# Optimization experiments

Measured on AMD Instinct MI355X. Metric: run time of the kernel, lower is better.

The kernel has to match this reference:

```python
import jax, jax.numpy as jnp
import numpy as np

HIDDEN = 1024  # must match init_kwargs hidden_size


def setup_inputs() -> dict:
    key = jax.random.key(0)
    k1, k2 = jax.random.split(key)
    B, SQ, SKV, D = 4, 4096, 4096, HIDDEN
    query = jax.random.normal(k1, (B, SQ, D), dtype=jnp.float32)
    key_value_states = jax.random.normal(k2, (B, SKV, D), dtype=jnp.float32)
    attention_mask = jnp.zeros((B, 1, SKV), dtype=jnp.float32)
    return {
        "query": query,
        "key_value_states": key_value_states,
        "attention_mask": attention_mask,
        "layer_idx": 0,
    }


def reference(query, key_value_states, attention_mask, layer_idx):
    # compression_rate = 1.0 + layer_idx/12*3 ; layer_idx=0 -> rate 1.0 (no compression)
    scale = 1.0 / jnp.sqrt(jnp.asarray(HIDDEN, dtype=query.dtype))
    # scores: [B, Sq, Skv]
    scores = jnp.einsum("bqd,bkd->bqk", query, key_value_states) * scale
    scores = scores + attention_mask
    attn = jax.nn.softmax(scores, axis=-1)
    # dropout is identity (eval / p=0)
    out = jnp.einsum("bqk,bkd->bqd", attn, key_value_states)
    return out, attn
```

## Files before the change

kernel.cpp:

```cpp
#include <hip/hip_runtime.h>
#include <stdint.h>

#define B_   4
#define SQ_  4096
#define SKV_ 4096
#define D_   1024

typedef __attribute__((ext_vector_type(4))) float f32x4;
typedef __attribute__((ext_vector_type(8))) short bf8_t;

__device__ __forceinline__ unsigned short f2bf(float f) {
    unsigned u = __float_as_uint(f);
    u += 0x7fff + ((u >> 16) & 1);
    return (unsigned short)(u >> 16);
}

__device__ __forceinline__ void gload_lds16(const void* g, void* l) {
    __builtin_amdgcn_global_load_lds(
        (const __attribute__((address_space(1))) unsigned int*)g,
        (__attribute__((address_space(3))) unsigned int*)l,
        16, 0, 0);
}

__device__ __forceinline__ void barrier_mem() {
    asm volatile("" ::: "memory");
    __builtin_amdgcn_s_barrier();
    asm volatile("" ::: "memory");
}

__global__ void cvt_f32_bf16_kernel(const float* __restrict__ in,
                                    unsigned short* __restrict__ out, int n4) {
    int stride = gridDim.x * blockDim.x;
    for (int i = blockIdx.x * blockDim.x + threadIdx.x; i < n4; i += stride) {
        float4 v = ((const float4*)in)[i];
        ushort4 o;
        o.x = f2bf(v.x); o.y = f2bf(v.y); o.z = f2bf(v.z); o.w = f2bf(v.w);
        ((ushort4*)out)[i] = o;
    }
}

__global__ void transpose_cvt_kernel(const float* __restrict__ V,
                                     unsigned short* __restrict__ VT) {
    __shared__ float tile[32][33];
    int b = blockIdx.z;
    const float* Vb = V + (size_t)b * SKV_ * D_;
    unsigned short* VTb = VT + (size_t)b * D_ * SKV_;
    int d0 = blockIdx.x * 32, k0 = blockIdx.y * 32;
    int x = threadIdx.x, y = threadIdx.y;
    #pragma unroll
    for (int i = 0; i < 4; ++i)
        tile[y + i * 8][x] = Vb[(size_t)(k0 + y + i * 8) * D_ + d0 + x];
    __syncthreads();
    #pragma unroll
    for (int i = 0; i < 4; ++i)
        VTb[(size_t)(d0 + y + i * 8) * SKV_ + k0 + x] = f2bf(tile[x][y + i * 8]);
}

__global__ __launch_bounds__(512, 2) void gemm256_nt_bf16_kernel(
    const unsigned short* __restrict__ A, int lda, size_t strideA,
    const unsigned short* __restrict__ Bm, int ldb, size_t strideB,
    float* __restrict__ C, int ldc, size_t strideC,
    int K, float scale, const float* __restrict__ mask)
{
    __shared__ __align__(16) unsigned char smem[131072];

    const int tid  = threadIdx.x;
    const int lane = tid & 63, wid = tid >> 6;
    const int wr = wid >> 2, wc = wid & 3;

    int lin  = blockIdx.y * gridDim.x + blockIdx.x;
    int q8   = (gridDim.x * gridDim.y) >> 3;
    int lin2 = (lin & 7) * q8 + (lin >> 3);
    int bn = lin2 % gridDim.x, bm = lin2 / gridDim.x;
    int bz = blockIdx.z;

    const char* Ab = (const char*)(A + (size_t)bz * strideA);
    const char* Bb = (const char*)(Bm + (size_t)bz * strideB);
    float* Cb = C + (size_t)bz * strideC;
    const int ldaB = lda * 2, ldbB = ldb * 2;

    const int srow = ((tid >> 6) * 16) + (tid & 15);
    const int scol = ((tid >> 4) & 3) * 16;
    const char* Apan = Ab + (size_t)(bm * 256 + srow) * ldaB + scol;
    const char* Bpan = Bb + (size_t)(bn * 256 + srow) * ldbB + scol;
    char* ldsA = (char*)smem;
    char* ldsB = (char*)smem + 65536;

    const char* aRd = (char*)smem + wr * 8192 + lane * 16;
    const char* bRd = (char*)smem + 65536 + wc * 4096 + lane * 16;

    f32x4 acc[8][4] = {};
    const int NT = K >> 6;

#define STAGE_A(tt, hh) do { \
    const char* s_ = Apan + (tt) * 128 + (hh) * 64; \
    char* d_ = ldsA + (((tt) & 1) * 32768) + (hh) * 16384 + tid * 16; \
    gload_lds16(s_, d_); \
    gload_lds16(s_ + (size_t)128 * ldaB, d_ + 8192); \
} while (0)
#define STAGE_B(tt, hh) do { \
    const char* s_ = Bpan + (tt) * 128 + (hh) * 64; \
    char* d_ = ldsB + (((tt) & 1) * 32768) + (hh) * 16384 + tid * 16; \
    gload_lds16(s_, d_); \
    gload_lds16(s_ + (size_t)128 * ldbB, d_ + 8192); \
} while (0)

    STAGE_A(0, 0); STAGE_A(0, 1); STAGE_B(0, 0); STAGE_B(0, 1);
    if (NT > 1) {
        STAGE_A(1, 0); STAGE_B(1, 0); STAGE_B(1, 1);
        asm volatile("s_waitcnt vmcnt(6)" ::: "memory");
    } else {
        asm volatile("s_waitcnt vmcnt(0)" ::: "memory");
    }
    barrier_mem();

    for (int t = 0; t < NT; ++t) {
        const int p = t & 1;
        const char* aT = aRd + p * 32768;
        const char* bT = bRd + p * 32768;
        bf8_t a0[8], a1[8], b0[4], b1[4];

        #pragma unroll
        for (int m = 0; m < 8; ++m) a0[m] = *(const bf8_t*)(aT + m * 1024);
        #pragma unroll
        for (int n = 0; n < 4; ++n) b0[n] = *(const bf8_t*)(bT + n * 1024);
        if (t + 1 < NT) STAGE_A(t + 1, 1);
        barrier_mem();
        __builtin_amdgcn_s_setprio(1);
        #pragma unroll
        for (int m = 0; m < 4; ++m)
            #pragma unroll
            for (int n = 0; n < 4; ++n)
                acc[m][n] = __builtin_amdgcn_mfma_f32_16x16x32_bf16(a0[m], b0[n], acc[m][n], 0, 0, 0);
        __builtin_amdgcn_s_setprio(0);
        barrier_mem();

        #pragma unroll
        for (int n = 0; n < 4; ++n) b1[n] = *(const bf8_t*)(bT + 16384 + n * 1024);
        if (t + 2 < NT) STAGE_A(t + 2, 0);
        barrier_mem();
        __builtin_amdgcn_s_setprio(1);
        #pragma unroll
        for (int m = 0; m < 4; ++m)
            #pragma unroll
            for (int n = 0; n < 4; ++n)
                acc[m + 4][n] = __builtin_amdgcn_mfma_f32_16x16x32_bf16(a0[m + 4], b0[n], acc[m + 4][n], 0, 0, 0);
        __builtin_amdgcn_s_setprio(0);
        barrier_mem();

        #pragma unroll
        for (int m = 0; m < 8; ++m) a1[m] = *(const bf8_t*)(aT + 16384 + m * 1024);
        if (t + 2 < NT) STAGE_B(t + 2, 0);
        barrier_mem();
        __builtin_amdgcn_s_setprio(1);
        #pragma unroll
        for (int m = 0; m < 4; ++m)
            #pragma unroll
            for (int n = 0; n < 4; ++n)
                acc[m][n] = __builtin_amdgcn_mfma_f32_16x16x32_bf16(a1[m], b1[n], acc[m][n], 0, 0, 0);
        __builtin_amdgcn_s_setprio(0);
        barrier_mem();

        if (t + 2 < NT) STAGE_B(t + 2, 1);
        barrier_mem();
        __builtin_amdgcn_s_setprio(1);
        #pragma unroll
        for (int m = 0; m < 4; ++m)
            #pragma unroll
            for (int n = 0; n < 4; ++n)
                acc[m + 4][n] = __builtin_amdgcn_mfma_f32_16x16x32_bf16(a1[m + 4], b1[n], acc[m + 4][n], 0, 0, 0);
        __builtin_amdgcn_s_setprio(0);
        if (t + 2 < NT)      asm volatile("s_waitcnt vmcnt(6)" ::: "memory");
        else if (t + 1 < NT) asm volatile("s_waitcnt vmcnt(0)" ::: "memory");
        barrier_mem();
    }
#undef STAGE_A
#undef STAGE_B

    const int row0 = bm * 256 + wr * 128 + (lane >> 4) * 4;
    const int col0 = bn * 256 + wc * 64 + (lane & 15);
    const float* maskb = mask ? mask + (size_t)bz * SKV_ : nullptr;
    #pragma unroll
    for (int n = 0; n < 4; ++n) {
        int col = col0 + n * 16;
        float mk = maskb ? maskb[col] : 0.0f;
        #pragma unroll
        for (int m = 0; m < 8; ++m) {
            int row = row0 + m * 16;
            #pragma unroll
            for (int r = 0; r < 4; ++r)
                Cb[(size_t)(row + r) * ldc + col] = acc[m][n][r] * scale + mk;
        }
    }
}

__global__ __launch_bounds__(256) void softmax_kernel(float* __restrict__ scores,
                                                      unsigned short* __restrict__ abf) {
    __shared__ __align__(16) float buf[SKV_];
    __shared__ float red[4];
    size_t row = blockIdx.x;
    float* p = scores + row * SKV_;
    int t = threadIdx.x;

    float lmax = -3.4e38f;
    for (int i = t * 4; i < SKV_; i += 1024) {
        float4 v = *(const float4*)(p + i);
        *(float4*)&buf[i] = v;
        lmax = fmaxf(fmaxf(lmax, fmaxf(v.x, v.y)), fmaxf(v.z, v.w));
    }
    #pragma unroll
    for (int o = 32; o; o >>= 1) lmax = fmaxf(lmax, __shfl_down(lmax, o));
    if ((t & 63) == 0) red[t >> 6] = lmax;
    __syncthreads();
    float rmax = fmaxf(fmaxf(red[0], red[1]), fmaxf(red[2], red[3]));
    __syncthreads();

    float lsum = 0.f;
    for (int i = t * 4; i < SKV_; i += 1024) {
        float4 v = *(const float4*)&buf[i];
        v.x = __expf(v.x - rmax); v.y = __expf(v.y - rmax);
        v.z = __expf(v.z - rmax); v.w = __expf(v.w - rmax);
        *(float4*)&buf[i] = v;
        lsum += (v.x + v.y) + (v.z + v.w);
    }
    #pragma unroll
    for (int o = 32; o; o >>= 1) lsum += __shfl_down(lsum, o);
    if ((t & 63) == 0) red[t >> 6] = lsum;
    __syncthreads();
    float rinv = 1.0f / ((red[0] + red[1]) + (red[2] + red[3]));

    unsigned short* ab = abf ? abf + row * SKV_ : nullptr;
    for (int i = t * 4; i < SKV_; i += 1024) {
        float4 v = *(const float4*)&buf[i];
        v.x *= rinv; v.y *= rinv; v.z *= rinv; v.w *= rinv;
        *(float4*)(p + i) = v;
        if (ab) {
            ushort4 o;
            o.x = f2bf(v.x); o.y = f2bf(v.y); o.z = f2bf(v.z); o.w = f2bf(v.w);
            *(ushort4*)(ab + i) = o;
        }
    }
}

__global__ void naive_nt_kernel(const float* __restrict__ A, const float* __restrict__ Bm,
                                float* __restrict__ C, const float* __restrict__ mask,
                                int N, int K, float scale) {
    __shared__ float As[16][16], Bs[16][16];
    int b = blockIdx.z;
    const float* Ab = A + (size_t)b * SQ_ * K;
    const float* Bb = Bm + (size_t)b * N * K;
    float* Cb = C + (size_t)b * SQ_ * N;
    int tx = threadIdx.x, ty = threadIdx.y;
    int m = blockIdx.y * 16 + ty, n = blockIdx.x * 16 + tx;
    float acc = 0.f;
    for (int k0 = 0; k0 < K; k0 += 16) {
        As[ty][tx] = Ab[(size_t)m * K + k0 + tx];
        Bs[ty][tx] = Bb[(size_t)(blockIdx.x * 16 + ty) * K + k0 + tx];
        __syncthreads();
        #pragma unroll
        for (int kk = 0; kk < 16; ++kk) acc += As[ty][kk] * Bs[tx][kk];
        __syncthreads();
    }
    Cb[(size_t)m * N + n] = acc * scale + (mask ? mask[(size_t)b * SKV_ + n] : 0.f);
}

__global__ void naive_nn_kernel(const float* __restrict__ A, const float* __restrict__ Bm,
                                float* __restrict__ C, int N, int K) {
    __shared__ float As[16][16], Bs[16][17];
    int b = blockIdx.z;
    const float* Ab = A + (size_t)b * SQ_ * K;
    const float* Bb = Bm + (size_t)b * K * N;
    float* Cb = C + (size_t)b * SQ_ * N;
    int tx = threadIdx.x, ty = threadIdx.y;
    int m = blockIdx.y * 16 + ty, n = blockIdx.x * 16 + tx;
    float acc = 0.f;
    for (int k0 = 0; k0 < K; k0 += 16) {
        As[ty][tx] = Ab[(size_t)m * K + k0 + tx];
        Bs[ty][tx] = Bb[(size_t)(k0 + ty) * N + n];
        __syncthreads();
        #pragma unroll
        for (int kk = 0; kk < 16; ++kk) acc += As[ty][kk] * Bs[kk][tx];
        __syncthreads();
    }
    Cb[(size_t)m * N + n] = acc;
}

extern "C" void kernel_launch(void* const* d_in, const int* in_sizes, int n_in,
                              void* d_out, int out_size, void* d_ws, size_t ws_size,
                              hipStream_t stream) {
    const float* q    = (const float*)d_in[0];
    const float* kv   = (const float*)d_in[1];
    const float* mask = (const float*)d_in[2];

    float* out  = (float*)d_out;
    float* attn = out + (size_t)B_ * SQ_ * D_;
    const float scale = 0.03125f;

    size_t nQ    = (size_t)B_ * SQ_ * D_;
    size_t nKV   = (size_t)B_ * SKV_ * D_;
    size_t nAttn = (size_t)B_ * SQ_ * SKV_;
    size_t need  = (nQ + nKV + nKV + nAttn) * 2;

    if (ws_size >= need) {
        unsigned short* qbf  = (unsigned short*)d_ws;
        unsigned short* kbf  = qbf + nQ;
        unsigned short* vtbf = kbf + nKV;
        unsigned short* abf  = vtbf + nKV;

        cvt_f32_bf16_kernel<<<2048, 256, 0, stream>>>(q, qbf, (int)(nQ / 4));
        cvt_f32_bf16_kernel<<<2048, 256, 0, stream>>>(kv, kbf, (int)(nKV / 4));
        transpose_cvt_kernel<<<dim3(D_ / 32, SKV_ / 32, B_), dim3(32, 8), 0, stream>>>(kv, vtbf);

        gemm256_nt_bf16_kernel<<<dim3(SKV_ / 256, SQ_ / 256, B_), 512, 0, stream>>>(
            qbf, D_, (size_t)SQ_ * D_,
            kbf, D_, (size_t)SKV_ * D_,
            attn, SKV_, (size_t)SQ_ * SKV_,
            D_, scale, mask);

        softmax_kernel<<<B_ * SQ_, 256, 0, stream>>>(attn, abf);

        gemm256_nt_bf16_kernel<<<dim3(D_ / 256, SQ_ / 256, B_), 512, 0, stream>>>(
            abf, SKV_, (size_t)SQ_ * SKV_,
            vtbf, SKV_, (size_t)D_ * SKV_,
            out, D_, (size_t)SQ_ * D_,
            SKV_, 1.0f, nullptr);
    } else {
        naive_nt_kernel<<<dim3(SKV_ / 16, SQ_ / 16, B_), dim3(16, 16), 0, stream>>>(
            q, kv, attn, mask, SKV_, D_, scale);
        softmax_kernel<<<B_ * SQ_, 256, 0, stream>>>(attn, nullptr);
        naive_nn_kernel<<<dim3(D_ / 16, SQ_ / 16, B_), dim3(16, 16), 0, stream>>>(
            attn, kv, out, D_, SKV_);
    }
}
```

Before: 570.9 us.

## Store scores as fp16 in workspace, software-pipeline GEMM LDS reads, fuse K/V conversion

The QK^T GEMM now writes scaled and masked scores as fp16 into a workspace buffer instead of fp32 into the attention output. Softmax reads the fp16 buffer, writes the fp32 attention output, and overwrites the same buffer in place with bf16 probabilities for the PV GEMM. This halves the score write and read traffic. The GEMM main loop is restructured so each LDS fragment load is issued one MFMA group ahead, with adjusted vmcnt waits, and K conversion is fused into the V transpose kernel so kv is read once. The risks are fp16 range and precision loss on the scores, and a fragile hand-tuned wait pipeline.

```diff
diff --git a/kernel.cpp b/kernel.cpp
--- a/kernel.cpp
+++ b/kernel.cpp
@@ -1,4 +1,5 @@
 #include <hip/hip_runtime.h>
+#include <hip/hip_fp16.h>
 #include <stdint.h>
 
 #define B_   4
@@ -39,27 +40,33 @@
     }
 }
 
-__global__ void transpose_cvt_kernel(const float* __restrict__ V,
-                                     unsigned short* __restrict__ VT) {
+__global__ void cvtkv_kernel(const float* __restrict__ V,
+                             unsigned short* __restrict__ Kbf,
+                             unsigned short* __restrict__ VT) {
     __shared__ float tile[32][33];
     int b = blockIdx.z;
     const float* Vb = V + (size_t)b * SKV_ * D_;
+    unsigned short* Kb = Kbf + (size_t)b * SKV_ * D_;
     unsigned short* VTb = VT + (size_t)b * D_ * SKV_;
     int d0 = blockIdx.x * 32, k0 = blockIdx.y * 32;
     int x = threadIdx.x, y = threadIdx.y;
     #pragma unroll
-    for (int i = 0; i < 4; ++i)
-        tile[y + i * 8][x] = Vb[(size_t)(k0 + y + i * 8) * D_ + d0 + x];
+    for (int i = 0; i < 4; ++i) {
+        float v = Vb[(size_t)(k0 + y + i * 8) * D_ + d0 + x];
+        tile[y + i * 8][x] = v;
+        Kb[(size_t)(k0 + y + i * 8) * D_ + d0 + x] = f2bf(v);
+    }
     __syncthreads();
     #pragma unroll
     for (int i = 0; i < 4; ++i)
         VTb[(size_t)(d0 + y + i * 8) * SKV_ + k0 + x] = f2bf(tile[x][y + i * 8]);
 }
 
-__global__ __launch_bounds__(512, 2) void gemm256_nt_bf16_kernel(
+template<bool HALF_OUT>
+__global__ __launch_bounds__(512, 2) void gemm256_pipe_kernel(
     const unsigned short* __restrict__ A, int lda, size_t strideA,
     const unsigned short* __restrict__ Bm, int ldb, size_t strideB,
-    float* __restrict__ C, int ldc, size_t strideC,
+    void* __restrict__ Cv, int ldc, size_t strideC,
     int K, float scale, const float* __restrict__ mask)
 {
     __shared__ __align__(16) unsigned char smem[131072];
@@ -76,7 +83,6 @@
 
     const char* Ab = (const char*)(A + (size_t)bz * strideA);
     const char* Bb = (const char*)(Bm + (size_t)bz * strideB);
-    float* Cb = C + (size_t)bz * strideC;
     const int ldaB = lda * 2, ldbB = ldb * 2;
 
     const int srow = ((tid >> 6) * 16) + (tid & 15);
@@ -104,109 +110,137 @@
     gload_lds16(s_, d_); \
     gload_lds16(s_ + (size_t)128 * ldbB, d_ + 8192); \
 } while (0)
-
-    STAGE_A(0, 0); STAGE_A(0, 1); STAGE_B(0, 0); STAGE_B(0, 1);
+#define MFMA16(ACCBASE, AF, BF) do { \
+    __builtin_amdgcn_s_setprio(1); \
+    _Pragma("unroll") \
+    for (int m_ = 0; m_ < 4; ++m_) \
+        _Pragma("unroll") \
+        for (int n_ = 0; n_ < 4; ++n_) \
+            acc[(ACCBASE) + m_][n_] = __builtin_amdgcn_mfma_f32_16x16x32_bf16( \
+                AF[m_], BF[n_], acc[(ACCBASE) + m_][n_], 0, 0, 0); \
+    __builtin_amdgcn_s_setprio(0); \
+} while (0)
+
+    STAGE_B(0, 0); STAGE_A(0, 0); STAGE_B(0, 1); STAGE_A(0, 1);
     if (NT > 1) {
-        STAGE_A(1, 0); STAGE_B(1, 0); STAGE_B(1, 1);
-        asm volatile("s_waitcnt vmcnt(6)" ::: "memory");
+        STAGE_B(1, 0); STAGE_A(1, 0); STAGE_B(1, 1);
+        asm volatile("s_waitcnt vmcnt(10)" ::: "memory");
     } else {
         asm volatile("s_waitcnt vmcnt(0)" ::: "memory");
     }
     barrier_mem();
+
+    bf8_t aL[4], aH[4], bA[4], bB[4];
+    #pragma unroll
+    for (int m = 0; m < 4; ++m) aL[m] = *(const bf8_t*)(aRd + m * 1024);
+    #pragma unroll
+    for (int n = 0; n < 4; ++n) bA[n] = *(const bf8_t*)(bRd + n * 1024);
 
     for (int t = 0; t < NT; ++t) {
         const int p = t & 1;
         const char* aT = aRd + p * 32768;
         const char* bT = bRd + p * 32768;
-        bf8_t a0[8], a1[8], b0[4], b1[4];
-
-        #pragma unroll
-        for (int m = 0; m < 8; ++m) a0[m] = *(const bf8_t*)(aT + m * 1024);
-        #pragma unroll
-        for (int n = 0; n < 4; ++n) b0[n] = *(const bf8_t*)(bT + n * 1024);
+
         if (t + 1 < NT) STAGE_A(t + 1, 1);
         barrier_mem();
-        __builtin_amdgcn_s_setprio(1);
-        #pragma unroll
-        for (int m = 0; m < 4; ++m)
+        #pragma unroll
+        for (int m = 0; m < 4; ++m) aH[m] = *(const bf8_t*)(aT + (4 + m) * 1024);
+        MFMA16(0, aL, bA);
+        barrier_mem();
+
+        if (t == NT - 1) asm volatile("s_waitcnt vmcnt(0)" ::: "memory");
+        else             asm volatile("s_waitcnt vmcnt(8)" ::: "memory");
+        if (t + 2 < NT) STAGE_B(t + 2, 0);
+        barrier_mem();
+        #pragma unroll
+        for (int m = 0; m < 4; ++m) aL[m] = *(const bf8_t*)(aT + 16384 + m * 1024);
+        #pragma unroll
+        for (int n = 0; n < 4; ++n) bB[n] = *(const bf8_t*)(bT + 16384 + n * 1024);
+        MFMA16(4, aH, bA);
+        barrier_mem();
+
+        if (t + 2 < NT) STAGE_A(t + 2, 0);
+        barrier_mem();
+        #pragma unroll
+        for (int m = 0; m < 4; ++m) aH[m] = *(const bf8_t*)(aT + 16384 + (4 + m) * 1024);
+        MFMA16(0, aL, bB);
+        barrier_mem();
+
+        if (t + 2 < NT) {
+            asm volatile("s_waitcnt vmcnt(8)" ::: "memory");
+            STAGE_B(t + 2, 1);
+        } else if (t + 1 < NT) {
+            asm volatile("s_waitcnt vmcnt(4)" ::: "memory");
+        }
+        barrier_mem();
+        if (t + 1 < NT) {
+            const char* aTn = aRd + (p ^ 1) * 32768;
+            const char* bTn = bRd + (p ^ 1) * 32768;
             #pragma unroll
-            for (int n = 0; n < 4; ++n)
-                acc[m][n] = __builtin_amdgcn_mfma_f32_16x16x32_bf16(a0[m], b0[n], acc[m][n], 0, 0, 0);
-        __builtin_amdgcn_s_setprio(0);
-        barrier_mem();
-
-        #pragma unroll
-        for (int n = 0; n < 4; ++n) b1[n] = *(const bf8_t*)(bT + 16384 + n * 1024);
-        if (t + 2 < NT) STAGE_A(t + 2, 0);
-        barrier_mem();
-        __builtin_amdgcn_s_setprio(1);
-        #pragma unroll
-        for (int m = 0; m < 4; ++m)
+            for (int m = 0; m < 4; ++m) aL[m] = *(const bf8_t*)(aTn + m * 1024);
             #pragma unroll
-            for (int n = 0; n < 4; ++n)
-                acc[m + 4][n] = __builtin_amdgcn_mfma_f32_16x16x32_bf16(a0[m + 4], b0[n], acc[m + 4][n], 0, 0, 0);
-        __builtin_amdgcn_s_setprio(0);
-        barrier_mem();
-
-        #pragma unroll
-        for (int m = 0; m < 8; ++m) a1[m] = *(const bf8_t*)(aT + 16384 + m * 1024);
-        if (t + 2 < NT) STAGE_B(t + 2, 0);
-        barrier_mem();
-        __builtin_amdgcn_s_setprio(1);
-        #pragma unroll
-        for (int m = 0; m < 4; ++m)
-            #pragma unroll
-            for (int n = 0; n < 4; ++n)
-                acc[m][n] = __builtin_amdgcn_mfma_f32_16x16x32_bf16(a1[m], b1[n], acc[m][n], 0, 0, 0);
-        __builtin_amdgcn_s_setprio(0);
-        barrier_mem();
-
-        if (t + 2 < NT) STAGE_B(t + 2, 1);
-        barrier_mem();
-        __builtin_amdgcn_s_setprio(1);
-        #pragma unroll
-        for (int m = 0; m < 4; ++m)
-            #pragma unroll
-            for (int n = 0; n < 4; ++n)
-                acc[m + 4][n] = __builtin_amdgcn_mfma_f32_16x16x32_bf16(a1[m + 4], b1[n], acc[m + 4][n], 0, 0, 0);
-        __builtin_amdgcn_s_setprio(0);
-        if (t + 2 < NT)      asm volatile("s_waitcnt vmcnt(6)" ::: "memory");
-        else if (t + 1 < NT) asm volatile("s_waitcnt vmcnt(0)" ::: "memory");
+            for (int n = 0; n < 4; ++n) bA[n] = *(const bf8_t*)(bTn + n * 1024);
+        }
+        MFMA16(4, aH, bB);
         barrier_mem();
     }
 #undef STAGE_A
 #undef STAGE_B
+#undef MFMA16
 
     const int row0 = bm * 256 + wr * 128 + (lane >> 4) * 4;
     const int col0 = bn * 256 + wc * 64 + (lane & 15);
-    const float* maskb = mask ? mask + (size_t)bz * SKV_ : nullptr;
-    #pragma unroll
-    for (int n = 0; n < 4; ++n) {
-        int col = col0 + n * 16;
-        float mk = maskb ? maskb[col] : 0.0f;
-        #pragma unroll
-        for (int m = 0; m < 8; ++m) {
-            int row = row0 + m * 16;
+    if (HALF_OUT) {
+        __half* Ch = (__half*)Cv + (size_t)bz * strideC;
+        const float* maskb = mask + (size_t)bz * SKV_;
+        #pragma unroll
+        for (int n = 0; n < 4; ++n) {
+            int col = col0 + n * 16;
+            float mk = maskb[col];
             #pragma unroll
-            for (int r = 0; r < 4; ++r)
-                Cb[(size_t)(row + r) * ldc + col] = acc[m][n][r] * scale + mk;
+            for (int m = 0; m < 8; ++m) {
+                int row = row0 + m * 16;
+                #pragma unroll
+                for (int r = 0; r < 4; ++r)
+                    Ch[(size_t)(row + r) * ldc + col] = __float2half(acc[m][n][r] * scale + mk);
+            }
         }
-    }
-}
-
-__global__ __launch_bounds__(256) void softmax_kernel(float* __restrict__ scores,
-                                                      unsigned short* __restrict__ abf) {
+    } else {
+        float* Cf = (float*)Cv + (size_t)bz * strideC;
+        #pragma unroll
+        for (int n = 0; n < 4; ++n) {
+            int col = col0 + n * 16;
+            #pragma unroll
+            for (int m = 0; m < 8; ++m) {
+                int row = row0 + m * 16;
+                #pragma unroll
+                for (int r = 0; r < 4; ++r)
+                    Cf[(size_t)(row + r) * ldc + col] = acc[m][n][r];
+            }
+        }
+    }
+}
+
+__global__ __launch_bounds__(256) void softmax_kernel(unsigned short* __restrict__ s2,
+                                                      float* __restrict__ attn) {
     __shared__ __align__(16) float buf[SKV_];
     __shared__ float red[4];
     size_t row = blockIdx.x;
-    float* p = scores + row * SKV_;
+    unsigned short* p = s2 + row * SKV_;
+    float* ao = attn + row * SKV_;
     int t = threadIdx.x;
 
     float lmax = -3.4e38f;
-    for (int i = t * 4; i < SKV_; i += 1024) {
-        float4 v = *(const float4*)(p + i);
-        *(float4*)&buf[i] = v;
-        lmax = fmaxf(fmaxf(lmax, fmaxf(v.x, v.y)), fmaxf(v.z, v.w));
+    for (int i = t * 8; i < SKV_; i += 2048) {
+        uint4 hv = *(const uint4*)(p + i);
+        float2 f0 = __half22float2(*(__half2*)&hv.x);
+        float2 f1 = __half22float2(*(__half2*)&hv.y);
+        float2 f2 = __half22float2(*(__half2*)&hv.z);
+        float2 f3 = __half22float2(*(__half2*)&hv.w);
+        buf[i+0] = f0.x; buf[i+1] = f0.y; buf[i+2] = f1.x; buf[i+3] = f1.y;
+        buf[i+4] = f2.x; buf[i+5] = f2.y; buf[i+6] = f3.x; buf[i+7] = f3.y;
+        lmax = fmaxf(lmax, fmaxf(fmaxf(fmaxf(f0.x, f0.y), fmaxf(f1.x, f1.y)),
+                                 fmaxf(fmaxf(f2.x, f2.y), fmaxf(f3.x, f3.y))));
     }
     #pragma unroll
     for (int o = 32; o; o >>= 1) lmax = fmaxf(lmax, __shfl_down(lmax, o));
@@ -229,16 +263,56 @@
     __syncthreads();
     float rinv = 1.0f / ((red[0] + red[1]) + (red[2] + red[3]));
 
-    unsigned short* ab = abf ? abf + row * SKV_ : nullptr;
+    for (int i = t * 8; i < SKV_; i += 2048) {
+        float4 v0 = *(const float4*)&buf[i];
+        float4 v1 = *(const float4*)&buf[i + 4];
+        v0.x *= rinv; v0.y *= rinv; v0.z *= rinv; v0.w *= rinv;
+        v1.x *= rinv; v1.y *= rinv; v1.z *= rinv; v1.w *= rinv;
+        *(float4*)(ao + i) = v0;
+        *(float4*)(ao + i + 4) = v1;
+        ushort4 o0, o1;
+        o0.x = f2bf(v0.x); o0.y = f2bf(v0.y); o0.z = f2bf(v0.z); o0.w = f2bf(v0.w);
+        o1.x = f2bf(v1.x); o1.y = f2bf(v1.y); o1.z = f2bf(v1.z); o1.w = f2bf(v1.w);
+        *(ushort4*)(p + i) = o0;
+        *(ushort4*)(p + i + 4) = o1;
+    }
+}
+
+__global__ __launch_bounds__(256) void softmax_f32_kernel(float* __restrict__ scores) {
+    __shared__ __align__(16) float buf[SKV_];
+    __shared__ float red[4];
+    size_t row = blockIdx.x;
+    float* p = scores + row * SKV_;
+    int t = threadIdx.x;
+    float lmax = -3.4e38f;
+    for (int i = t * 4; i < SKV_; i += 1024) {
+        float4 v = *(const float4*)(p + i);
+        *(float4*)&buf[i] = v;
+        lmax = fmaxf(fmaxf(lmax, fmaxf(v.x, v.y)), fmaxf(v.z, v.w));
+    }
+    #pragma unroll
+    for (int o = 32; o; o >>= 1) lmax = fmaxf(lmax, __shfl_down(lmax, o));
+    if ((t & 63) == 0) red[t >> 6] = lmax;
+    __syncthreads();
+    float rmax = fmaxf(fmaxf(red[0], red[1]), fmaxf(red[2], red[3]));
+    __syncthreads();
+    float lsum = 0.f;
+    for (int i = t * 4; i < SKV_; i += 1024) {
+        float4 v = *(const float4*)&buf[i];
+        v.x = __expf(v.x - rmax); v.y = __expf(v.y - rmax);
+        v.z = __expf(v.z - rmax); v.w = __expf(v.w - rmax);
+        *(float4*)&buf[i] = v;
+        lsum += (v.x + v.y) + (v.z + v.w);
+    }
+    #pragma unroll
+    for (int o = 32; o; o >>= 1) lsum += __shfl_down(lsum, o);
+    if ((t & 63) == 0) red[t >> 6] = lsum;
+    __syncthreads();
+    float rinv = 1.0f / ((red[0] + red[1]) + (red[2] + red[3]));
     for (int i = t * 4; i < SKV_; i += 1024) {
         float4 v = *(const float4*)&buf[i];
         v.x *= rinv; v.y *= rinv; v.z *= rinv; v.w *= rinv;
         *(float4*)(p + i) = v;
-        if (ab) {
-            ushort4 o;
-            o.x = f2bf(v.x); o.y = f2bf(v.y); o.z = f2bf(v.z); o.w = f2bf(v.w);
-            *(ushort4*)(ab + i) = o;
-        }
     }
 }
 
@@ -305,29 +379,28 @@
         unsigned short* qbf  = (unsigned short*)d_ws;
         unsigned short* kbf  = qbf + nQ;
         unsigned short* vtbf = kbf + nKV;
-        unsigned short* abf  = vtbf + nKV;
+        unsigned short* s2   = vtbf + nKV;
 
         cvt_f32_bf16_kernel<<<2048, 256, 0, stream>>>(q, qbf, (int)(nQ / 4));
-        cvt_f32_bf16_kernel<<<2048, 256, 0, stream>>>(kv, kbf, (int)(nKV / 4));
-        transpose_cvt_kernel<<<dim3(D_ / 32, SKV_ / 32, B_), dim3(32, 8), 0, stream>>>(kv, vtbf);
-
-        gemm256_nt_bf16_kernel<<<dim3(SKV_ / 256, SQ_ / 256, B_), 512, 0, stream>>>(
+        cvtkv_kernel<<<dim3(D_ / 32, SKV_ / 32, B_), dim3(32, 8), 0, stream>>>(kv, kbf, vtbf);
+
+        gemm256_pipe_kernel<true><<<dim3(SKV_ / 256, SQ_ / 256, B_), 512, 0, stream>>>(
             qbf, D_, (size_t)SQ_ * D_,
             kbf, D_, (size_t)SKV_ * D_,
-            attn, SKV_, (size_t)SQ_ * SKV_,
+            (void*)s2, SKV_, (size_t)SQ_ * SKV_,
             D_, scale, mask);
 
-        softmax_kernel<<<B_ * SQ_, 256, 0, stream>>>(attn, abf);
-
-        gemm256_nt_bf16_kernel<<<dim3(D_ / 256, SQ_ / 256, B_), 512, 0, stream>>>(
-            abf, SKV_, (size_t)SQ_ * SKV_,
+        softmax_kernel<<<B_ * SQ_, 256, 0, stream>>>(s2, attn);
+
+        gemm256_pipe_kernel<false><<<dim3(D_ / 256, SQ_ / 256, B_), 512, 0, stream>>>(
+            s2, SKV_, (size_t)SQ_ * SKV_,
             vtbf, SKV_, (size_t)D_ * SKV_,
-            out, D_, (size_t)SQ_ * D_,
+            (void*)out, D_, (size_t)SQ_ * D_,
             SKV_, 1.0f, nullptr);
     } else {
         naive_nt_kernel<<<dim3(SKV_ / 16, SQ_ / 16, B_), dim3(16, 16), 0, stream>>>(
             q, kv, attn, mask, SKV_, D_, scale);
-        softmax_kernel<<<B_ * SQ_, 256, 0, stream>>>(attn, nullptr);
+        softmax_f32_kernel<<<B_ * SQ_, 256, 0, stream>>>(attn);
         naive_nn_kernel<<<dim3(D_ / 16, SQ_ / 16, B_), dim3(16, 16), 0, stream>>>(
             attn, kv, out, D_, SKV_);
     }
```

Result: faster. 482.8 us (-15.4%).
